# Kernel optimization log

Hardware: AMD Instinct MI355X
Metric: run time of the kernel (lower is better)

Reference implementation:

```python
import jax, jax.numpy as jnp
import numpy as np

B, N, D, H, DH, L = 2, 1024, 1024, 16, 64, 6
INNER = D * 4 * 2 // 3  # GEGLU inner dim = 2730
SCALE = DH ** -0.5


def _ln(x, g, b):
    m = jnp.mean(x, -1, keepdims=True)
    v = jnp.var(x, -1, keepdims=True)
    return (x - m) / jnp.sqrt(v + 1e-5) * g + b


def _stable_softmax(t, alpha=1024.0):  # alpha = 32**2
    t = t / alpha
    t = t - jax.lax.stop_gradient(jnp.max(t, -1, keepdims=True))
    return jax.nn.softmax(t * alpha, axis=-1)


def setup_inputs() -> dict:
    key = jax.random.key(0)
    ks = jax.random.split(key, 10)
    rn = lambda k, s, sc=0.02: jax.random.normal(k, s, jnp.float32) * sc
    return {
        'x': jax.random.normal(ks[0], (B, N, D), jnp.float32),
        'attn_pre_g': jnp.ones((L, D)), 'attn_pre_b': jnp.zeros((L, D)),
        'attn_post_g': jnp.ones((L, D)), 'attn_post_b': jnp.zeros((L, D)),
        'Wq': rn(ks[1], (L, D, H * DH)), 'Wkv': rn(ks[2], (L, D, 2 * H * DH)),
        'Wo': rn(ks[3], (L, H * DH, D)), 'bo': jnp.zeros((L, D)),
        'null_k': rn(ks[4], (L, H, DH), 1.0), 'null_v': rn(ks[5], (L, H, DH), 1.0),
        'talk': rn(ks[6], (L, H, H), H ** -0.5),
        'ff_pre_g': jnp.ones((L, D)), 'ff_pre_b': jnp.zeros((L, D)),
        'ff_post_g': jnp.ones((L, D)), 'ff_post_b': jnp.zeros((L, D)),
        'W1': rn(ks[7], (L, D, 2 * INNER)), 'b1': jnp.zeros((L, 2 * INNER)),
        'W2': rn(ks[8], (L, INNER, D)), 'b2': jnp.zeros((L, D)),
        'final_g': jnp.ones((D,)), 'final_b': jnp.zeros((D,)),
    }


def _forward(x, attn_pre_g, attn_pre_b, attn_post_g, attn_post_b, Wq, Wkv, Wo, bo,
             null_k, null_v, talk, ff_pre_g, ff_pre_b, ff_post_g, ff_post_b,
             W1, b1, W2, b2, final_g, final_b):
    b, n, _ = x.shape
    neg = -jnp.finfo(x.dtype).max
    causal = jnp.triu(jnp.ones((n, n + 1), bool), 2)  # null kv slot at j=0 never masked
    for l in range(L):
        # --- talking-heads attention, sandwich-normed ---
        h = _ln(x, attn_pre_g[l], attn_pre_b[l])
        q = (h @ Wq[l]).reshape(b, n, H, DH).transpose(0, 2, 1, 3)
        k, v = jnp.split(h @ Wkv[l], 2, -1)
        k = k.reshape(b, n, H, DH).transpose(0, 2, 1, 3)
        v = v.reshape(b, n, H, DH).transpose(0, 2, 1, 3)
        nk = jnp.broadcast_to(null_k[l][None, :, None, :], (b, H, 1, DH))
        nv = jnp.broadcast_to(null_v[l][None, :, None, :], (b, H, 1, DH))
        k = jnp.concatenate([nk, k], 2)  # [b,H,n+1,DH]
        v = jnp.concatenate([nv, v], 2)
        sim = jnp.einsum('bhid,bhjd->bhij', q * SCALE, k)
        sim = jnp.where(causal, neg, sim)
        a = _stable_softmax(sim)
        a = jnp.einsum('gh,bhij->bgij', talk[l], a)  # 1x1 Conv2d over head channel
        o = jnp.einsum('bhij,bhjd->bhid', a, v).transpose(0, 2, 1, 3).reshape(b, n, H * DH)
        o = o @ Wo[l] + bo[l]
        x = x + _ln(o, attn_post_g[l], attn_post_b[l])
        # --- GEGLU feedforward, sandwich-normed ---
        h = _ln(x, ff_pre_g[l], ff_pre_b[l])
        u = h @ W1[l] + b1[l]
        ua, ug = jnp.split(u, 2, -1)
        o = (ua * jax.nn.gelu(ug, approximate=False)) @ W2[l] + b2[l]
        x = x + _ln(o, ff_post_g[l], ff_post_b[l])
    # StableLayerNorm
    x = x / jax.lax.stop_gradient(jnp.max(x, -1, keepdims=True))
    return _ln(x, final_g, final_b)


def reference(x, attn_pre_g, attn_pre_b, attn_post_g, attn_post_b, Wq, Wkv, Wo, bo,
              null_k, null_v, talk, ff_pre_g, ff_pre_b, ff_post_g, ff_post_b,
              W1, b1, W2, b2, final_g, final_b):
    return _forward(x, attn_pre_g, attn_pre_b, attn_post_g, attn_post_b, Wq, Wkv, Wo, bo,
                    null_k, null_v, talk, ff_pre_g, ff_pre_b, ff_post_g, ff_post_b,
                    W1, b1, W2, b2, final_g, final_b)
```

## Files before the change

### kernel.cpp

```cpp
#include <hip/hip_runtime.h>
#include <hip/hip_bf16.h>
#include <float.h>
#include <math.h>


#define N_SEQ 1024
#define DMODEL 1024
#define NH 16
#define DH 64
#define NLAYER 6
#define FF_INNER 2730
#define K2PAD 2752
#define PSTRIDE 1028

typedef float f32x4 __attribute__((ext_vector_type(4)));
typedef short s16x8 __attribute__((ext_vector_type(8)));
typedef unsigned long long u64;

__device__ __forceinline__ ushort f2bf(float f) {
  return __builtin_bit_cast(ushort, __float2bfloat16(f));
}
__device__ __forceinline__ u64 pack4(float a, float b, float c, float d) {
  return (u64)f2bf(a) | ((u64)f2bf(b) << 16) | ((u64)f2bf(c) << 32) |
         ((u64)f2bf(d) << 48);
}
#define GLD_LDS16(g, l)                                                        \
  __builtin_amdgcn_global_load_lds(                                            \
      (const __attribute__((address_space(1))) void*)(g),                      \
      (__attribute__((address_space(3))) void*)(l), 16, 0, 0)

__device__ __forceinline__ float wave_sum(float v) {
#pragma unroll
  for (int o = 32; o > 0; o >>= 1) v += __shfl_xor(v, o, 64);
  return v;
}
__device__ __forceinline__ float wave_max(float v) {
#pragma unroll
  for (int o = 32; o > 0; o >>= 1) v = fmaxf(v, __shfl_xor(v, o, 64));
  return v;
}
__device__ __forceinline__ float block_sum(float v, float* s) {
  v = wave_sum(v);
  __syncthreads();
  if ((threadIdx.x & 63) == 0) s[threadIdx.x >> 6] = v;
  __syncthreads();
  return s[0] + s[1] + s[2] + s[3];
}
__device__ __forceinline__ float block_max(float v, float* s) {
  v = wave_max(v);
  __syncthreads();
  if ((threadIdx.x & 63) == 0) s[threadIdx.x >> 6] = v;
  __syncthreads();
  return fmaxf(fmaxf(s[0], s[1]), fmaxf(s[2], s[3]));
}

__global__ __launch_bounds__(256) void ln_res_kernel(const float* __restrict__ in,
                                                     const float* __restrict__ gw,
                                                     const float* __restrict__ bw,
                                                     float* __restrict__ out) {
  __shared__ float red[4];
  const int row = blockIdx.x, t = threadIdx.x;
  float4 v = *(const float4*)(in + (size_t)row * DMODEL + t * 4);
  float mean = block_sum(v.x + v.y + v.z + v.w, red) * (1.0f / DMODEL);
  float4 d = make_float4(v.x - mean, v.y - mean, v.z - mean, v.w - mean);
  float var = block_sum(d.x * d.x + d.y * d.y + d.z * d.z + d.w * d.w, red) * (1.0f / DMODEL);
  float rstd = rsqrtf(var + 1e-5f);
  float4 g4 = *(const float4*)(gw + t * 4);
  float4 b4 = *(const float4*)(bw + t * 4);
  float* q = out + (size_t)row * DMODEL + t * 4;
  float4 xv = *(float4*)q;
  xv.x += d.x * rstd * g4.x + b4.x;
  xv.y += d.y * rstd * g4.y + b4.y;
  xv.z += d.z * rstd * g4.z + b4.z;
  xv.w += d.w * rstd * g4.w + b4.w;
  *(float4*)q = xv;
}

__global__ __launch_bounds__(256) void ln_bf16_kernel(const float* __restrict__ in,
                                                      const float* __restrict__ gw,
                                                      const float* __restrict__ bw,
                                                      ushort* __restrict__ out) {
  __shared__ float red[4];
  const int row = blockIdx.x, t = threadIdx.x;
  float4 v = *(const float4*)(in + (size_t)row * DMODEL + t * 4);
  float mean = block_sum(v.x + v.y + v.z + v.w, red) * (1.0f / DMODEL);
  float4 d = make_float4(v.x - mean, v.y - mean, v.z - mean, v.w - mean);
  float var = block_sum(d.x * d.x + d.y * d.y + d.z * d.z + d.w * d.w, red) * (1.0f / DMODEL);
  float rstd = rsqrtf(var + 1e-5f);
  float4 g4 = *(const float4*)(gw + t * 4);
  float4 b4 = *(const float4*)(bw + t * 4);
  *(u64*)(out + (size_t)row * DMODEL + t * 4) =
      pack4(d.x * rstd * g4.x + b4.x, d.y * rstd * g4.y + b4.y,
            d.z * rstd * g4.z + b4.z, d.w * rstd * g4.w + b4.w);
}

__global__ __launch_bounds__(256) void final_kernel(const float* __restrict__ in,
                                                    const float* __restrict__ gw,
                                                    const float* __restrict__ bw,
                                                    float* __restrict__ out) {
  __shared__ float red[4];
  const int row = blockIdx.x, t = threadIdx.x;
  float4 v = *(const float4*)(in + (size_t)row * DMODEL + t * 4);
  float mx = block_max(fmaxf(fmaxf(v.x, v.y), fmaxf(v.z, v.w)), red);
  float4 y = make_float4(v.x / mx, v.y / mx, v.z / mx, v.w / mx);
  float mean = block_sum(y.x + y.y + y.z + y.w, red) * (1.0f / DMODEL);
  float4 d = make_float4(y.x - mean, y.y - mean, y.z - mean, y.w - mean);
  float var = block_sum(d.x * d.x + d.y * d.y + d.z * d.z + d.w * d.w, red) * (1.0f / DMODEL);
  float rstd = rsqrtf(var + 1e-5f);
  float4 g4 = *(const float4*)(gw + t * 4);
  float4 b4 = *(const float4*)(bw + t * 4);
  float4 r = make_float4(d.x * rstd * g4.x + b4.x, d.y * rstd * g4.y + b4.y,
                         d.z * rstd * g4.z + b4.z, d.w * rstd * g4.w + b4.w);
  *(float4*)(out + (size_t)row * DMODEL + t * 4) = r;
}

__global__ __launch_bounds__(256) void cvtT_kernel(const float* __restrict__ W,
                                                   ushort* __restrict__ Wt,
                                                   int K, int N, int Kpad) {
  __shared__ float tile[32][33];
  const int n0 = blockIdx.x * 32, k0 = blockIdx.y * 32;
  const int tr = threadIdx.x >> 3, tc4 = (threadIdx.x & 7) * 4;
  int gk = k0 + tr;
  float4 v = make_float4(0, 0, 0, 0);
  if (gk < K) {
    if (n0 + tc4 + 3 < N) {
      v = *(const float4*)(W + (size_t)gk * N + n0 + tc4);
    } else {
      if (n0 + tc4 + 0 < N) v.x = W[(size_t)gk * N + n0 + tc4 + 0];
      if (n0 + tc4 + 1 < N) v.y = W[(size_t)gk * N + n0 + tc4 + 1];
      if (n0 + tc4 + 2 < N) v.z = W[(size_t)gk * N + n0 + tc4 + 2];
      if (n0 + tc4 + 3 < N) v.w = W[(size_t)gk * N + n0 + tc4 + 3];
    }
  }
  tile[tr][tc4 + 0] = v.x; tile[tr][tc4 + 1] = v.y;
  tile[tr][tc4 + 2] = v.z; tile[tr][tc4 + 3] = v.w;
  __syncthreads();
  *(u64*)(Wt + (size_t)(n0 + tr) * Kpad + k0 + tc4) =
      pack4(tile[tc4 + 0][tr], tile[tc4 + 1][tr], tile[tc4 + 2][tr], tile[tc4 + 3][tr]);
}

__global__ __launch_bounds__(256) void gemm_bf16(const ushort* __restrict__ A,
                                                 const ushort* __restrict__ Bt,
                                                 const float* __restrict__ bias,
                                                 float* __restrict__ C,
                                                 int N, int K, int lda, int ldb) {
  __shared__ __align__(16) ushort Al[128 * 32];
  __shared__ __align__(16) ushort Bl[128 * 32];
  const int n0 = blockIdx.x * 128, m0 = blockIdx.y * 128;
  const int t = threadIdx.x, lane = t & 63, w = t >> 6;
  const int wm = w >> 1, wn = w & 1;

  f32x4 acc[4][4];
#pragma unroll
  for (int i = 0; i < 4; i++)
#pragma unroll
    for (int j = 0; j < 4; j++) acc[i][j] = (f32x4){0.f, 0.f, 0.f, 0.f};

  const int sm = t >> 2, sk = (t & 3) * 8;
  const ushort* ga0 = A + (size_t)(m0 + sm) * lda + sk;
  const ushort* ga1 = ga0 + (size_t)64 * lda;
  const ushort* gb0 = Bt + (size_t)(n0 + sm) * ldb + sk;
  const ushort* gb1 = gb0 + (size_t)64 * ldb;
  ushort* la0 = &Al[t * 8];
  ushort* la1 = &Al[2048 + t * 8];
  ushort* lb0 = &Bl[t * 8];
  ushort* lb1 = &Bl[2048 + t * 8];

  const int kk = (lane >> 4) * 8;
  const int rA = wm * 64 + (lane & 15);
  const int rB = wn * 64 + (lane & 15);

  for (int k0 = 0; k0 < K; k0 += 32) {
    GLD_LDS16(ga0 + k0, la0);
    GLD_LDS16(ga1 + k0, la1);
    GLD_LDS16(gb0 + k0, lb0);
    GLD_LDS16(gb1 + k0, lb1);
    __syncthreads();
    s16x8 fa[4], fb[4];
#pragma unroll
    for (int mi = 0; mi < 4; mi++)
      fa[mi] = *(const s16x8*)&Al[(rA + mi * 16) * 32 + kk];
#pragma unroll
    for (int ni = 0; ni < 4; ni++)
      fb[ni] = *(const s16x8*)&Bl[(rB + ni * 16) * 32 + kk];
#pragma unroll
    for (int mi = 0; mi < 4; mi++)
#pragma unroll
      for (int ni = 0; ni < 4; ni++)
        acc[mi][ni] = __builtin_amdgcn_mfma_f32_16x16x32_bf16(
            fa[mi], fb[ni], acc[mi][ni], 0, 0, 0);
    __syncthreads();
  }

  const int crow = m0 + wm * 64 + (lane >> 4) * 4;
  const int ccol = n0 + wn * 64 + (lane & 15);
#pragma unroll
  for (int ni = 0; ni < 4; ni++) {
    int gc = ccol + ni * 16;
    if (gc >= N) continue;
    float bv = bias ? bias[gc] : 0.f;
#pragma unroll
    for (int mi = 0; mi < 4; mi++)
#pragma unroll
      for (int r = 0; r < 4; r++)
        C[(size_t)(crow + mi * 16 + r) * N + gc] = acc[mi][ni][r] + bv;
  }
}

__global__ __launch_bounds__(256) void scores_kernel(const float* __restrict__ q,
                                                     const float* __restrict__ kv,
                                                     const float* __restrict__ nullk,
                                                     float* __restrict__ probs, int b) {
  __shared__ float Qs[64][68];
  __shared__ float Ks[64][68];
  const int h = blockIdx.z, i0 = blockIdx.y * 64, j0 = blockIdx.x * 64;
  const int t = threadIdx.x, tx = t & 15, ty = t >> 4;
#pragma unroll
  for (int r = 0; r < 4; r++) {
    int f = t + r * 256;
    int i = f >> 4, d4 = (f & 15) << 2;
    float4 v = *(const float4*)(q + ((size_t)(b * N_SEQ) + i0 + i) * DMODEL + h * DH + d4);
    Qs[d4 + 0][i] = v.x; Qs[d4 + 1][i] = v.y; Qs[d4 + 2][i] = v.z; Qs[d4 + 3][i] = v.w;
  }
#pragma unroll
  for (int r = 0; r < 4; r++) {
    int f = t + r * 256;
    int j = f >> 4, d4 = (f & 15) << 2;
    int jg = j0 + j;
    float4 v = make_float4(0, 0, 0, 0);
    if (jg == 0)
      v = *(const float4*)(nullk + h * DH + d4);
    else if (jg < N_SEQ + 1)
      v = *(const float4*)(kv + ((size_t)(b * N_SEQ) + jg - 1) * 2048 + h * DH + d4);
    Ks[d4 + 0][j] = v.x; Ks[d4 + 1][j] = v.y; Ks[d4 + 2][j] = v.z; Ks[d4 + 3][j] = v.w;
  }
  __syncthreads();
  float acc[4][4];
#pragma unroll
  for (int i = 0; i < 4; i++)
#pragma unroll
    for (int j = 0; j < 4; j++) acc[i][j] = 0.f;
#pragma unroll 16
  for (int d = 0; d < 64; d++) {
    float av[4], bv[4];
    *(float4*)av = *(const float4*)&Qs[d][ty * 4];
    *(float4*)bv = *(const float4*)&Ks[d][tx * 4];
#pragma unroll
    for (int i = 0; i < 4; i++)
#pragma unroll
      for (int j = 0; j < 4; j++) acc[i][j] = fmaf(av[i], bv[j], acc[i][j]);
  }
#pragma unroll
  for (int ii = 0; ii < 4; ii++) {
    int i = i0 + ty * 4 + ii;
#pragma unroll
    for (int jj = 0; jj < 4; jj++) {
      int j = j0 + tx * 4 + jj;
      if (j < N_SEQ + 1) {
        float s = acc[ii][jj] * 0.125f;
        if (j > i + 1) s = -FLT_MAX;
        probs[((size_t)h * N_SEQ + i) * PSTRIDE + j] = s;
      }
    }
  }
}

__global__ __launch_bounds__(256) void softmax_kernel(float* __restrict__ probs) {
  __shared__ float red[4];
  const int row = blockIdx.x;
  float* p = probs + (size_t)row * PSTRIDE;
  const int t = threadIdx.x;
  float v[5];
#pragma unroll
  for (int c = 0; c < 5; c++) {
    int j = t + c * 256;
    v[c] = (j < N_SEQ + 1) ? p[j] : -FLT_MAX;
  }
  float m = fmaxf(fmaxf(fmaxf(v[0], v[1]), fmaxf(v[2], v[3])), v[4]);
  m = block_max(m, red);
  float s = 0.f;
#pragma unroll
  for (int c = 0; c < 5; c++) {
    v[c] = expf(v[c] - m);
    s += v[c];
  }
  s = block_sum(s, red);
#pragma unroll
  for (int c = 0; c < 5; c++) {
    int j = t + c * 256;
    if (j < N_SEQ + 1) p[j] = v[c] / s;
  }
}

__global__ __launch_bounds__(256) void mix_kernel(float* __restrict__ probs,
                                                  const float* __restrict__ talk) {
  __shared__ float tk[256];
  const int i = blockIdx.x;
  tk[threadIdx.x] = talk[threadIdx.x];
  __syncthreads();
  for (int j = threadIdx.x; j < N_SEQ + 1; j += 256) {
    float a[16];
#pragma unroll
    for (int hh = 0; hh < 16; hh++) a[hh] = probs[((size_t)hh * N_SEQ + i) * PSTRIDE + j];
#pragma unroll
    for (int g = 0; g < 16; g++) {
      float s = 0.f;
#pragma unroll
      for (int hh = 0; hh < 16; hh++) s = fmaf(tk[g * 16 + hh], a[hh], s);
      probs[((size_t)g * N_SEQ + i) * PSTRIDE + j] = s;
    }
  }
}

__global__ __launch_bounds__(256) void av_kernel(const float* __restrict__ probs,
                                                 const float* __restrict__ kv,
                                                 const float* __restrict__ nullv,
                                                 ushort* __restrict__ o, int b) {
  __shared__ float Ps[32][68];
  __shared__ float Vs[32][68];
  const int h = blockIdx.y, i0 = blockIdx.x * 64;
  const int t = threadIdx.x, tx = t & 15, ty = t >> 4;
  float acc[4][4];
#pragma unroll
  for (int i = 0; i < 4; i++)
#pragma unroll
    for (int j = 0; j < 4; j++) acc[i][j] = 0.f;

  for (int j0 = 0; j0 < N_SEQ + 1; j0 += 32) {
#pragma unroll
    for (int r = 0; r < 2; r++) {
      int f = t + r * 256;
      int i = f >> 3, j4 = (f & 7) << 2;
      const float* src = probs + ((size_t)h * N_SEQ + i0 + i) * PSTRIDE + j0 + j4;
      float e[4];
      if (j0 + j4 + 3 < N_SEQ + 1) {
        float4 v = *(const float4*)src;
        e[0] = v.x; e[1] = v.y; e[2] = v.z; e[3] = v.w;
      } else {
#pragma unroll
        for (int c = 0; c < 4; c++) e[c] = (j0 + j4 + c < N_SEQ + 1) ? src[c] : 0.f;
      }
      Ps[j4 + 0][i] = e[0]; Ps[j4 + 1][i] = e[1]; Ps[j4 + 2][i] = e[2]; Ps[j4 + 3][i] = e[3];
    }
#pragma unroll
    for (int r = 0; r < 2; r++) {
      int f = t + r * 256;
      int j = f >> 4, d4 = (f & 15) << 2;
      int jg = j0 + j;
      float4 v = make_float4(0, 0, 0, 0);
      if (jg == 0)
        v = *(const float4*)(nullv + h * DH + d4);
      else if (jg < N_SEQ + 1)
        v = *(const float4*)(kv + ((size_t)(b * N_SEQ) + jg - 1) * 2048 + 1024 + h * DH + d4);
      *(float4*)&Vs[j][d4] = v;
    }
    __syncthreads();
#pragma unroll 8
    for (int jj = 0; jj < 32; jj++) {
      float av[4], bv[4];
      *(float4*)av = *(const float4*)&Ps[jj][ty * 4];
      *(float4*)bv = *(const float4*)&Vs[jj][tx * 4];
#pragma unroll
      for (int i = 0; i < 4; i++)
#pragma unroll
        for (int j = 0; j < 4; j++) acc[i][j] = fmaf(av[i], bv[j], acc[i][j]);
    }
    __syncthreads();
  }
#pragma unroll
  for (int ii = 0; ii < 4; ii++) {
    *(u64*)(o + ((size_t)(b * N_SEQ) + i0 + ty * 4 + ii) * DMODEL + h * DH + tx * 4) =
        pack4(acc[ii][0], acc[ii][1], acc[ii][2], acc[ii][3]);
  }
}

__global__ __launch_bounds__(256) void geglu_kernel(const float* __restrict__ u,
                                                    ushort* __restrict__ gg) {
  const int i = blockIdx.y;
  const int j = blockIdx.x * 256 + threadIdx.x;
  if (j < K2PAD) {
    float r = 0.f;
    if (j < FF_INNER) {
      float a = u[(size_t)i * (2 * FF_INNER) + j];
      float x = u[(size_t)i * (2 * FF_INNER) + FF_INNER + j];
      r = a * 0.5f * x * (1.0f + erff(x * 0.70710678118654752f));
    }
    gg[(size_t)i * K2PAD + j] = f2bf(r);
  }
}

extern "C" void kernel_launch(void* const* d_in, const int* in_sizes, int n_in,
                              void* d_out, int out_size, void* d_ws, size_t ws_size,
                              hipStream_t stream) {
  const float* xin        = (const float*)d_in[0];
  const float* attn_pre_g = (const float*)d_in[1];
  const float* attn_pre_b = (const float*)d_in[2];
  const float* attn_post_g= (const float*)d_in[3];
  const float* attn_post_b= (const float*)d_in[4];
  const float* Wq         = (const float*)d_in[5];
  const float* Wkv        = (const float*)d_in[6];
  const float* Wo         = (const float*)d_in[7];
  const float* bo         = (const float*)d_in[8];
  const float* null_k     = (const float*)d_in[9];
  const float* null_v     = (const float*)d_in[10];
  const float* talk       = (const float*)d_in[11];
  const float* ff_pre_g   = (const float*)d_in[12];
  const float* ff_pre_b   = (const float*)d_in[13];
  const float* ff_post_g  = (const float*)d_in[14];
  const float* ff_post_b  = (const float*)d_in[15];
  const float* W1         = (const float*)d_in[16];
  const float* b1         = (const float*)d_in[17];
  const float* W2         = (const float*)d_in[18];
  const float* b2         = (const float*)d_in[19];
  const float* final_g    = (const float*)d_in[20];
  const float* final_b    = (const float*)d_in[21];

  if (ws_size < (size_t)29425664 * sizeof(float)) return;

  float* ws = (float*)d_ws;
  float*  X   = ws;
  ushort* Hbf = (ushort*)(X + (size_t)2097152);
  float*  Q   = (float*)(Hbf) + 1048576;
  float*  KV  = Q + (size_t)2097152;
  ushort* Obf = (ushort*)(KV + (size_t)4194304);
  float*  P2  = (float*)(Obf) + 1048576;
  float*  PR  = P2 + (size_t)2097152;
  float*  PROBS = PR;
  float*  U     = PR;
  ushort* GGbf  = (ushort*)(PR + 11182080);
  ushort* Wt    = (ushort*)(PR + 14000128);

  hipMemcpyAsync(X, xin, (size_t)2097152 * sizeof(float),
                 hipMemcpyDeviceToDevice, stream);

  dim3 blk(256);
  for (int l = 0; l < NLAYER; l++) {
    ln_bf16_kernel<<<2048, blk, 0, stream>>>(X, attn_pre_g + l * 1024, attn_pre_b + l * 1024, Hbf);
    cvtT_kernel<<<dim3(32, 32), blk, 0, stream>>>(Wq + (size_t)l * 1048576, Wt, 1024, 1024, 1024);
    gemm_bf16<<<dim3(8, 16), blk, 0, stream>>>(Hbf, Wt, nullptr, Q, 1024, 1024, 1024, 1024);
    cvtT_kernel<<<dim3(64, 32), blk, 0, stream>>>(Wkv + (size_t)l * 2097152, Wt, 1024, 2048, 1024);
    gemm_bf16<<<dim3(16, 16), blk, 0, stream>>>(Hbf, Wt, nullptr, KV, 2048, 1024, 1024, 1024);
    for (int b = 0; b < 2; b++) {
      scores_kernel<<<dim3(17, 16, 16), blk, 0, stream>>>(Q, KV, null_k + l * NH * DH, PROBS, b);
      softmax_kernel<<<16384, blk, 0, stream>>>(PROBS);
      mix_kernel<<<1024, blk, 0, stream>>>(PROBS, talk + l * 256);
      av_kernel<<<dim3(16, 16), blk, 0, stream>>>(PROBS, KV, null_v + l * NH * DH, Obf, b);
    }
    cvtT_kernel<<<dim3(32, 32), blk, 0, stream>>>(Wo + (size_t)l * 1048576, Wt, 1024, 1024, 1024);
    gemm_bf16<<<dim3(8, 16), blk, 0, stream>>>(Obf, Wt, bo + l * 1024, P2, 1024, 1024, 1024, 1024);
    ln_res_kernel<<<2048, blk, 0, stream>>>(P2, attn_post_g + l * 1024, attn_post_b + l * 1024, X);

    ln_bf16_kernel<<<2048, blk, 0, stream>>>(X, ff_pre_g + l * 1024, ff_pre_b + l * 1024, Hbf);
    cvtT_kernel<<<dim3(172, 32), blk, 0, stream>>>(W1 + (size_t)l * 5591040, Wt, 1024, 5460, 1024);
    gemm_bf16<<<dim3(43, 16), blk, 0, stream>>>(Hbf, Wt, b1 + l * 5460, U, 5460, 1024, 1024, 1024);
    geglu_kernel<<<dim3(11, 2048), blk, 0, stream>>>(U, GGbf);
    cvtT_kernel<<<dim3(32, 86), blk, 0, stream>>>(W2 + (size_t)l * 2795520, Wt, 2730, 1024, K2PAD);
    gemm_bf16<<<dim3(8, 16), blk, 0, stream>>>(GGbf, Wt, b2 + l * 1024, P2, 1024, K2PAD, K2PAD, K2PAD);
    ln_res_kernel<<<2048, blk, 0, stream>>>(P2, ff_post_g + l * 1024, ff_post_b + l * 1024, X);
  }
  final_kernel<<<2048, blk, 0, stream>>>(X, final_g, final_b, (float*)d_out);
}
```

Before: 3.978 ms.

## Move attention to bf16 MFMA with fused causal softmax and talking-heads mix

```diff
diff --git a/kernel.cpp b/kernel.cpp
--- a/kernel.cpp
+++ b/kernel.cpp
@@ -6,12 +6,12 @@
 
 #define N_SEQ 1024
 #define DMODEL 1024
-#define NH 16
-#define DH 64
 #define NLAYER 6
 #define FF_INNER 2730
 #define K2PAD 2752
-#define PSTRIDE 1028
+#define PSTR 1028
+#define PBSTR 1056
+#define KHROWS 1152
 
 typedef float f32x4 __attribute__((ext_vector_type(4)));
 typedef short s16x8 __attribute__((ext_vector_type(8)));
@@ -19,6 +19,9 @@
 
 __device__ __forceinline__ ushort f2bf(float f) {
   return __builtin_bit_cast(ushort, __float2bfloat16(f));
+}
+__device__ __forceinline__ float bf2f(ushort u) {
+  union { unsigned i; float f; } x; x.i = ((unsigned)u) << 16; return x.f;
 }
 __device__ __forceinline__ u64 pack4(float a, float b, float c, float d) {
   return (u64)f2bf(a) | ((u64)f2bf(b) << 16) | ((u64)f2bf(c) << 32) |
@@ -139,10 +142,11 @@
       pack4(tile[tc4 + 0][tr], tile[tc4 + 1][tr], tile[tc4 + 2][tr], tile[tc4 + 3][tr]);
 }
 
+template <int OBF>
 __global__ __launch_bounds__(256) void gemm_bf16(const ushort* __restrict__ A,
                                                  const ushort* __restrict__ Bt,
                                                  const float* __restrict__ bias,
-                                                 float* __restrict__ C,
+                                                 void* __restrict__ Cv,
                                                  int N, int K, int lda, int ldb) {
   __shared__ __align__(16) ushort Al[128 * 32];
   __shared__ __align__(16) ushort Bl[128 * 32];
@@ -202,187 +206,244 @@
 #pragma unroll
     for (int mi = 0; mi < 4; mi++)
 #pragma unroll
-      for (int r = 0; r < 4; r++)
-        C[(size_t)(crow + mi * 16 + r) * N + gc] = acc[mi][ni][r] + bv;
-  }
-}
-
-__global__ __launch_bounds__(256) void scores_kernel(const float* __restrict__ q,
-                                                     const float* __restrict__ kv,
-                                                     const float* __restrict__ nullk,
-                                                     float* __restrict__ probs, int b) {
-  __shared__ float Qs[64][68];
-  __shared__ float Ks[64][68];
-  const int h = blockIdx.z, i0 = blockIdx.y * 64, j0 = blockIdx.x * 64;
-  const int t = threadIdx.x, tx = t & 15, ty = t >> 4;
-#pragma unroll
-  for (int r = 0; r < 4; r++) {
-    int f = t + r * 256;
-    int i = f >> 4, d4 = (f & 15) << 2;
-    float4 v = *(const float4*)(q + ((size_t)(b * N_SEQ) + i0 + i) * DMODEL + h * DH + d4);
-    Qs[d4 + 0][i] = v.x; Qs[d4 + 1][i] = v.y; Qs[d4 + 2][i] = v.z; Qs[d4 + 3][i] = v.w;
-  }
-#pragma unroll
-  for (int r = 0; r < 4; r++) {
-    int f = t + r * 256;
-    int j = f >> 4, d4 = (f & 15) << 2;
-    int jg = j0 + j;
-    float4 v = make_float4(0, 0, 0, 0);
-    if (jg == 0)
-      v = *(const float4*)(nullk + h * DH + d4);
-    else if (jg < N_SEQ + 1)
-      v = *(const float4*)(kv + ((size_t)(b * N_SEQ) + jg - 1) * 2048 + h * DH + d4);
-    Ks[d4 + 0][j] = v.x; Ks[d4 + 1][j] = v.y; Ks[d4 + 2][j] = v.z; Ks[d4 + 3][j] = v.w;
-  }
-  __syncthreads();
-  float acc[4][4];
+      for (int r = 0; r < 4; r++) {
+        float val = acc[mi][ni][r] + bv;
+        size_t off = (size_t)(crow + mi * 16 + r) * N + gc;
+        if (OBF) ((ushort*)Cv)[off] = f2bf(val);
+        else     ((float*)Cv)[off]  = val;
+      }
+  }
+}
+
+__global__ __launch_bounds__(256) void prep_kv(const ushort* __restrict__ KVbf,
+                                               const float* __restrict__ nk,
+                                               const float* __restrict__ nv,
+                                               ushort* __restrict__ Kh,
+                                               ushort* __restrict__ Vt) {
+  const int b = blockIdx.x >> 4, h = blockIdx.x & 15;
+  const int t = threadIdx.x;
+  ushort* khb = Kh + (size_t)(b * 16 + h) * KHROWS * 64;
+  for (int idx = t; idx < KHROWS * 16; idx += 256) {
+    int j = idx >> 4, c4 = (idx & 15) * 4;
+    u64 v = 0;
+    if (j == 0) {
+      v = pack4(nk[h * 64 + c4], nk[h * 64 + c4 + 1],
+                nk[h * 64 + c4 + 2], nk[h * 64 + c4 + 3]);
+    } else if (j <= N_SEQ) {
+      v = *(const u64*)&KVbf[(size_t)(b * N_SEQ + j - 1) * 2048 + h * 64 + c4];
+    }
+    *(u64*)&khb[j * 64 + c4] = v;
+  }
+  ushort* vtb = Vt + (size_t)(b * 16 + h) * 64 * PBSTR;
+  for (int idx = t; idx < PBSTR * 16; idx += 256) {
+    int j = idx >> 4, d4 = (idx & 15) * 4;
+    ushort e0 = 0, e1 = 0, e2 = 0, e3 = 0;
+    if (j == 0) {
+      e0 = f2bf(nv[h * 64 + d4]);     e1 = f2bf(nv[h * 64 + d4 + 1]);
+      e2 = f2bf(nv[h * 64 + d4 + 2]); e3 = f2bf(nv[h * 64 + d4 + 3]);
+    } else if (j <= N_SEQ) {
+      u64 v = *(const u64*)&KVbf[(size_t)(b * N_SEQ + j - 1) * 2048 + 1024 + h * 64 + d4];
+      e0 = (ushort)v; e1 = (ushort)(v >> 16); e2 = (ushort)(v >> 32); e3 = (ushort)(v >> 48);
+    }
+    vtb[(d4 + 0) * PBSTR + j] = e0;
+    vtb[(d4 + 1) * PBSTR + j] = e1;
+    vtb[(d4 + 2) * PBSTR + j] = e2;
+    vtb[(d4 + 3) * PBSTR + j] = e3;
+  }
+}
+
+__global__ __launch_bounds__(256) void scores_mfma(const ushort* __restrict__ Qbf,
+                                                   const ushort* __restrict__ Kh,
+                                                   float* __restrict__ probs,
+                                                   int b, int ihalf) {
+  const int tj = blockIdx.x, til = blockIdx.y, h = blockIdx.z;
+  const int ti = ihalf * 4 + til;
+  const int m0 = ti * 128, n0 = tj * 128;
+  if (n0 > m0 + 128) return;
+  __shared__ __align__(16) ushort Al[128 * 32];
+  __shared__ __align__(16) ushort Bl[128 * 32];
+  const int t = threadIdx.x, lane = t & 63, w = t >> 6;
+  const int wm = w >> 1, wn = w & 1;
+
+  f32x4 acc[4][4];
 #pragma unroll
   for (int i = 0; i < 4; i++)
 #pragma unroll
-    for (int j = 0; j < 4; j++) acc[i][j] = 0.f;
-#pragma unroll 16
-  for (int d = 0; d < 64; d++) {
-    float av[4], bv[4];
-    *(float4*)av = *(const float4*)&Qs[d][ty * 4];
-    *(float4*)bv = *(const float4*)&Ks[d][tx * 4];
-#pragma unroll
-    for (int i = 0; i < 4; i++)
-#pragma unroll
-      for (int j = 0; j < 4; j++) acc[i][j] = fmaf(av[i], bv[j], acc[i][j]);
-  }
-#pragma unroll
-  for (int ii = 0; ii < 4; ii++) {
-    int i = i0 + ty * 4 + ii;
-#pragma unroll
-    for (int jj = 0; jj < 4; jj++) {
-      int j = j0 + tx * 4 + jj;
-      if (j < N_SEQ + 1) {
-        float s = acc[ii][jj] * 0.125f;
-        if (j > i + 1) s = -FLT_MAX;
-        probs[((size_t)h * N_SEQ + i) * PSTRIDE + j] = s;
+    for (int j = 0; j < 4; j++) acc[i][j] = (f32x4){0.f, 0.f, 0.f, 0.f};
+
+  const int sm = t >> 2, sk = (t & 3) * 8;
+  const ushort* ga0 = Qbf + (size_t)(b * N_SEQ + m0 + sm) * DMODEL + h * 64 + sk;
+  const ushort* ga1 = ga0 + (size_t)64 * DMODEL;
+  const ushort* gb0 = Kh + ((size_t)(b * 16 + h) * KHROWS + n0 + sm) * 64 + sk;
+  const ushort* gb1 = gb0 + (size_t)64 * 64;
+  ushort* la0 = &Al[t * 8];
+  ushort* la1 = &Al[2048 + t * 8];
+  ushort* lb0 = &Bl[t * 8];
+  ushort* lb1 = &Bl[2048 + t * 8];
+
+  const int kk = (lane >> 4) * 8;
+  const int rA = wm * 64 + (lane & 15);
+  const int rB = wn * 64 + (lane & 15);
+
+#pragma unroll
+  for (int k0 = 0; k0 < 64; k0 += 32) {
+    GLD_LDS16(ga0 + k0, la0);
+    GLD_LDS16(ga1 + k0, la1);
+    GLD_LDS16(gb0 + k0, lb0);
+    GLD_LDS16(gb1 + k0, lb1);
+    __syncthreads();
+    s16x8 fa[4], fb[4];
+#pragma unroll
+    for (int mi = 0; mi < 4; mi++)
+      fa[mi] = *(const s16x8*)&Al[(rA + mi * 16) * 32 + kk];
+#pragma unroll
+    for (int ni = 0; ni < 4; ni++)
+      fb[ni] = *(const s16x8*)&Bl[(rB + ni * 16) * 32 + kk];
+#pragma unroll
+    for (int mi = 0; mi < 4; mi++)
+#pragma unroll
+      for (int ni = 0; ni < 4; ni++)
+        acc[mi][ni] = __builtin_amdgcn_mfma_f32_16x16x32_bf16(
+            fa[mi], fb[ni], acc[mi][ni], 0, 0, 0);
+    __syncthreads();
+  }
+
+  const int crow = m0 + wm * 64 + (lane >> 4) * 4;
+  const int ccol = n0 + wn * 64 + (lane & 15);
+#pragma unroll
+  for (int ni = 0; ni < 4; ni++) {
+    int gc = ccol + ni * 16;
+    if (gc >= PSTR) continue;
+#pragma unroll
+    for (int mi = 0; mi < 4; mi++)
+#pragma unroll
+      for (int r = 0; r < 4; r++) {
+        int ig = crow + mi * 16 + r;
+        probs[((size_t)h * 512 + (ig & 511)) * PSTR + gc] = acc[mi][ni][r] * 0.125f;
+      }
+  }
+}
+
+__global__ __launch_bounds__(256) void smmix_kernel(const float* __restrict__ probs,
+                                                    const float* __restrict__ talk,
+                                                    ushort* __restrict__ PB, int ihalf) {
+  __shared__ __align__(16) float sl[16][PSTR];
+  __shared__ float tk[16][16];
+  __shared__ float ms[16], rls[16];
+  const int il = blockIdx.x;
+  const int ig = ihalf * 512 + il;
+  const int jmax = ig + 2;
+  const int t = threadIdx.x;
+  tk[t >> 4][t & 15] = talk[t];
+  const int nch = (jmax + 3) >> 2;
+  for (int idx = t; idx < 16 * nch; idx += 256) {
+    int h = idx / nch, c = idx - h * nch;
+    *(float4*)&sl[h][c * 4] = *(const float4*)&probs[((size_t)h * 512 + il) * PSTR + c * 4];
+  }
+  __syncthreads();
+  {
+    const int h = t >> 4, l16 = t & 15;
+    float m = -FLT_MAX;
+    for (int j = l16; j < jmax; j += 16) m = fmaxf(m, sl[h][j]);
+#pragma unroll
+    for (int o = 1; o < 16; o <<= 1) m = fmaxf(m, __shfl_xor(m, o, 16));
+    float s = 0.f;
+    for (int j = l16; j < jmax; j += 16) s += expf(sl[h][j] - m);
+#pragma unroll
+    for (int o = 1; o < 16; o <<= 1) s += __shfl_xor(s, o, 16);
+    if (l16 == 0) { ms[h] = m; rls[h] = 1.0f / s; }
+  }
+  __syncthreads();
+  for (int idx = t; idx < 16 * 257; idx += 256) {
+    int h = idx / 257, c = idx - h * 257;
+    float4 v = *(float4*)&sl[h][c * 4];
+    float m = ms[h], rl = rls[h];
+    int j = c * 4;
+    v.x = (j + 0 < jmax) ? expf(v.x - m) * rl : 0.f;
+    v.y = (j + 1 < jmax) ? expf(v.y - m) * rl : 0.f;
+    v.z = (j + 2 < jmax) ? expf(v.z - m) * rl : 0.f;
+    v.w = (j + 3 < jmax) ? expf(v.w - m) * rl : 0.f;
+    *(float4*)&sl[h][c * 4] = v;
+  }
+  __syncthreads();
+  for (int idx = t; idx < 16 * (PBSTR / 4); idx += 256) {
+    int g = idx / (PBSTR / 4), c = idx - g * (PBSTR / 4);
+    float ax = 0.f, ay = 0.f, az = 0.f, aw = 0.f;
+    if (c < 257) {
+#pragma unroll
+      for (int h = 0; h < 16; h++) {
+        float4 p = *(float4*)&sl[h][c * 4];
+        float wgh = tk[g][h];
+        ax += wgh * p.x; ay += wgh * p.y; az += wgh * p.z; aw += wgh * p.w;
       }
     }
-  }
-}
-
-__global__ __launch_bounds__(256) void softmax_kernel(float* __restrict__ probs) {
-  __shared__ float red[4];
-  const int row = blockIdx.x;
-  float* p = probs + (size_t)row * PSTRIDE;
-  const int t = threadIdx.x;
-  float v[5];
-#pragma unroll
-  for (int c = 0; c < 5; c++) {
-    int j = t + c * 256;
-    v[c] = (j < N_SEQ + 1) ? p[j] : -FLT_MAX;
-  }
-  float m = fmaxf(fmaxf(fmaxf(v[0], v[1]), fmaxf(v[2], v[3])), v[4]);
-  m = block_max(m, red);
-  float s = 0.f;
-#pragma unroll
-  for (int c = 0; c < 5; c++) {
-    v[c] = expf(v[c] - m);
-    s += v[c];
-  }
-  s = block_sum(s, red);
-#pragma unroll
-  for (int c = 0; c < 5; c++) {
-    int j = t + c * 256;
-    if (j < N_SEQ + 1) p[j] = v[c] / s;
-  }
-}
-
-__global__ __launch_bounds__(256) void mix_kernel(float* __restrict__ probs,
-                                                  const float* __restrict__ talk) {
-  __shared__ float tk[256];
-  const int i = blockIdx.x;
-  tk[threadIdx.x] = talk[threadIdx.x];
-  __syncthreads();
-  for (int j = threadIdx.x; j < N_SEQ + 1; j += 256) {
-    float a[16];
-#pragma unroll
-    for (int hh = 0; hh < 16; hh++) a[hh] = probs[((size_t)hh * N_SEQ + i) * PSTRIDE + j];
-#pragma unroll
-    for (int g = 0; g < 16; g++) {
-      float s = 0.f;
-#pragma unroll
-      for (int hh = 0; hh < 16; hh++) s = fmaf(tk[g * 16 + hh], a[hh], s);
-      probs[((size_t)g * N_SEQ + i) * PSTRIDE + j] = s;
-    }
-  }
-}
-
-__global__ __launch_bounds__(256) void av_kernel(const float* __restrict__ probs,
-                                                 const float* __restrict__ kv,
-                                                 const float* __restrict__ nullv,
-                                                 ushort* __restrict__ o, int b) {
-  __shared__ float Ps[32][68];
-  __shared__ float Vs[32][68];
-  const int h = blockIdx.y, i0 = blockIdx.x * 64;
-  const int t = threadIdx.x, tx = t & 15, ty = t >> 4;
-  float acc[4][4];
-#pragma unroll
-  for (int i = 0; i < 4; i++)
-#pragma unroll
-    for (int j = 0; j < 4; j++) acc[i][j] = 0.f;
-
-  for (int j0 = 0; j0 < N_SEQ + 1; j0 += 32) {
-#pragma unroll
-    for (int r = 0; r < 2; r++) {
-      int f = t + r * 256;
-      int i = f >> 3, j4 = (f & 7) << 2;
-      const float* src = probs + ((size_t)h * N_SEQ + i0 + i) * PSTRIDE + j0 + j4;
-      float e[4];
-      if (j0 + j4 + 3 < N_SEQ + 1) {
-        float4 v = *(const float4*)src;
-        e[0] = v.x; e[1] = v.y; e[2] = v.z; e[3] = v.w;
-      } else {
-#pragma unroll
-        for (int c = 0; c < 4; c++) e[c] = (j0 + j4 + c < N_SEQ + 1) ? src[c] : 0.f;
-      }
-      Ps[j4 + 0][i] = e[0]; Ps[j4 + 1][i] = e[1]; Ps[j4 + 2][i] = e[2]; Ps[j4 + 3][i] = e[3];
-    }
-#pragma unroll
-    for (int r = 0; r < 2; r++) {
-      int f = t + r * 256;
-      int j = f >> 4, d4 = (f & 15) << 2;
-      int jg = j0 + j;
-      float4 v = make_float4(0, 0, 0, 0);
-      if (jg == 0)
-        v = *(const float4*)(nullv + h * DH + d4);
-      else if (jg < N_SEQ + 1)
-        v = *(const float4*)(kv + ((size_t)(b * N_SEQ) + jg - 1) * 2048 + 1024 + h * DH + d4);
-      *(float4*)&Vs[j][d4] = v;
-    }
+    *(u64*)&PB[((size_t)g * N_SEQ + ig) * PBSTR + c * 4] = pack4(ax, ay, az, aw);
+  }
+}
+
+__global__ __launch_bounds__(256) void av_mfma(const ushort* __restrict__ PB,
+                                               const ushort* __restrict__ Vt,
+                                               ushort* __restrict__ Obf, int b) {
+  __shared__ __align__(16) ushort Al[64 * 32];
+  __shared__ __align__(16) ushort Bl[64 * 32];
+  const int m0 = blockIdx.x * 64, g = blockIdx.y;
+  const int t = threadIdx.x, lane = t & 63, w = t >> 6;
+  const int wm = w >> 1, wn = w & 1;
+  f32x4 acc[2][2];
+#pragma unroll
+  for (int i = 0; i < 2; i++)
+#pragma unroll
+    for (int j = 0; j < 2; j++) acc[i][j] = (f32x4){0.f, 0.f, 0.f, 0.f};
+
+  const int sm = t >> 2, sk = (t & 3) * 8;
+  const ushort* ga = PB + ((size_t)g * N_SEQ + m0 + sm) * PBSTR + sk;
+  const ushort* gb = Vt + ((size_t)(b * 16 + g) * 64 + sm) * PBSTR + sk;
+  ushort* la = &Al[t * 8];
+  ushort* lb = &Bl[t * 8];
+
+  const int kk = (lane >> 4) * 8;
+  const int rA = wm * 32 + (lane & 15);
+  const int rB = wn * 32 + (lane & 15);
+
+  for (int k0 = 0; k0 < PBSTR; k0 += 32) {
+    GLD_LDS16(ga + k0, la);
+    GLD_LDS16(gb + k0, lb);
     __syncthreads();
-#pragma unroll 8
-    for (int jj = 0; jj < 32; jj++) {
-      float av[4], bv[4];
-      *(float4*)av = *(const float4*)&Ps[jj][ty * 4];
-      *(float4*)bv = *(const float4*)&Vs[jj][tx * 4];
-#pragma unroll
-      for (int i = 0; i < 4; i++)
-#pragma unroll
-        for (int j = 0; j < 4; j++) acc[i][j] = fmaf(av[i], bv[j], acc[i][j]);
-    }
+    s16x8 fa[2], fb[2];
+    fa[0] = *(const s16x8*)&Al[rA * 32 + kk];
+    fa[1] = *(const s16x8*)&Al[(rA + 16) * 32 + kk];
+    fb[0] = *(const s16x8*)&Bl[rB * 32 + kk];
+    fb[1] = *(const s16x8*)&Bl[(rB + 16) * 32 + kk];
+#pragma unroll
+    for (int mi = 0; mi < 2; mi++)
+#pragma unroll
+      for (int ni = 0; ni < 2; ni++)
+        acc[mi][ni] = __builtin_amdgcn_mfma_f32_16x16x32_bf16(
+            fa[mi], fb[ni], acc[mi][ni], 0, 0, 0);
     __syncthreads();
   }
-#pragma unroll
-  for (int ii = 0; ii < 4; ii++) {
-    *(u64*)(o + ((size_t)(b * N_SEQ) + i0 + ty * 4 + ii) * DMODEL + h * DH + tx * 4) =
-        pack4(acc[ii][0], acc[ii][1], acc[ii][2], acc[ii][3]);
-  }
-}
-
-__global__ __launch_bounds__(256) void geglu_kernel(const float* __restrict__ u,
+
+  const int crow = m0 + wm * 32 + (lane >> 4) * 4;
+  const int ccol = wn * 32 + (lane & 15);
+#pragma unroll
+  for (int ni = 0; ni < 2; ni++)
+#pragma unroll
+    for (int mi = 0; mi < 2; mi++)
+#pragma unroll
+      for (int r = 0; r < 4; r++)
+        Obf[(size_t)(b * N_SEQ + crow + mi * 16 + r) * DMODEL + g * 64 + ccol + ni * 16] =
+            f2bf(acc[mi][ni][r]);
+}
+
+__global__ __launch_bounds__(256) void geglu_kernel(const ushort* __restrict__ u,
                                                     ushort* __restrict__ gg) {
   const int i = blockIdx.y;
   const int j = blockIdx.x * 256 + threadIdx.x;
   if (j < K2PAD) {
     float r = 0.f;
     if (j < FF_INNER) {
-      float a = u[(size_t)i * (2 * FF_INNER) + j];
-      float x = u[(size_t)i * (2 * FF_INNER) + FF_INNER + j];
+      float a = bf2f(u[(size_t)i * (2 * FF_INNER) + j]);
+      float x = bf2f(u[(size_t)i * (2 * FF_INNER) + FF_INNER + j]);
       r = a * 0.5f * x * (1.0f + erff(x * 0.70710678118654752f));
     }
     gg[(size_t)i * K2PAD + j] = f2bf(r);
@@ -415,20 +476,23 @@
   const float* final_g    = (const float*)d_in[20];
   const float* final_b    = (const float*)d_in[21];
 
-  if (ws_size < (size_t)29425664 * sizeof(float)) return;
+  if (ws_size < (size_t)28217344 * sizeof(float)) return;
 
   float* ws = (float*)d_ws;
-  float*  X   = ws;
-  ushort* Hbf = (ushort*)(X + (size_t)2097152);
-  float*  Q   = (float*)(Hbf) + 1048576;
-  float*  KV  = Q + (size_t)2097152;
-  ushort* Obf = (ushort*)(KV + (size_t)4194304);
-  float*  P2  = (float*)(Obf) + 1048576;
-  float*  PR  = P2 + (size_t)2097152;
-  float*  PROBS = PR;
-  float*  U     = PR;
-  ushort* GGbf  = (ushort*)(PR + 11182080);
-  ushort* Wt    = (ushort*)(PR + 14000128);
+  float*  X    = ws;
+  ushort* Hbf  = (ushort*)(ws + 2097152);
+  ushort* Obf  = Hbf;
+  ushort* Qbf  = (ushort*)(ws + 3145728);
+  ushort* KVbf = (ushort*)(ws + 4194304);
+  ushort* PB   = (ushort*)(ws + 4194304);
+  float*  P2   = ws + 12632064;
+  ushort* Kh   = (ushort*)(ws + 14729216);
+  ushort* Vt   = (ushort*)(ws + 15908864);
+  float*  BIG  = ws + 16990208;
+  float*  PROBS = BIG;
+  ushort* Ubf   = (ushort*)BIG;
+  ushort* GGbf  = (ushort*)(BIG + 5591040);
+  ushort* Wt    = (ushort*)(BIG + 8409088);
 
   hipMemcpyAsync(X, xin, (size_t)2097152 * sizeof(float),
                  hipMemcpyDeviceToDevice, stream);
@@ -437,25 +501,27 @@
   for (int l = 0; l < NLAYER; l++) {
     ln_bf16_kernel<<<2048, blk, 0, stream>>>(X, attn_pre_g + l * 1024, attn_pre_b + l * 1024, Hbf);
     cvtT_kernel<<<dim3(32, 32), blk, 0, stream>>>(Wq + (size_t)l * 1048576, Wt, 1024, 1024, 1024);
-    gemm_bf16<<<dim3(8, 16), blk, 0, stream>>>(Hbf, Wt, nullptr, Q, 1024, 1024, 1024, 1024);
+    gemm_bf16<1><<<dim3(8, 16), blk, 0, stream>>>(Hbf, Wt, nullptr, Qbf, 1024, 1024, 1024, 1024);
     cvtT_kernel<<<dim3(64, 32), blk, 0, stream>>>(Wkv + (size_t)l * 2097152, Wt, 1024, 2048, 1024);
-    gemm_bf16<<<dim3(16, 16), blk, 0, stream>>>(Hbf, Wt, nullptr, KV, 2048, 1024, 1024, 1024);
+    gemm_bf16<1><<<dim3(16, 16), blk, 0, stream>>>(Hbf, Wt, nullptr, KVbf, 2048, 1024, 1024, 1024);
+    prep_kv<<<32, blk, 0, stream>>>(KVbf, null_k + l * 1024, null_v + l * 1024, Kh, Vt);
     for (int b = 0; b < 2; b++) {
-      scores_kernel<<<dim3(17, 16, 16), blk, 0, stream>>>(Q, KV, null_k + l * NH * DH, PROBS, b);
-      softmax_kernel<<<16384, blk, 0, stream>>>(PROBS);
-      mix_kernel<<<1024, blk, 0, stream>>>(PROBS, talk + l * 256);
-      av_kernel<<<dim3(16, 16), blk, 0, stream>>>(PROBS, KV, null_v + l * NH * DH, Obf, b);
+      for (int ih = 0; ih < 2; ih++) {
+        scores_mfma<<<dim3(9, 4, 16), blk, 0, stream>>>(Qbf, Kh, PROBS, b, ih);
+        smmix_kernel<<<512, blk, 0, stream>>>(PROBS, talk + l * 256, PB, ih);
+      }
+      av_mfma<<<dim3(16, 16), blk, 0, stream>>>(PB, Vt, Obf, b);
     }
     cvtT_kernel<<<dim3(32, 32), blk, 0, stream>>>(Wo + (size_t)l * 1048576, Wt, 1024, 1024, 1024);
-    gemm_bf16<<<dim3(8, 16), blk, 0, stream>>>(Obf, Wt, bo + l * 1024, P2, 1024, 1024, 1024, 1024);
+    gemm_bf16<0><<<dim3(8, 16), blk, 0, stream>>>(Obf, Wt, bo + l * 1024, P2, 1024, 1024, 1024, 1024);
     ln_res_kernel<<<2048, blk, 0, stream>>>(P2, attn_post_g + l * 1024, attn_post_b + l * 1024, X);
 
     ln_bf16_kernel<<<2048, blk, 0, stream>>>(X, ff_pre_g + l * 1024, ff_pre_b + l * 1024, Hbf);
     cvtT_kernel<<<dim3(172, 32), blk, 0, stream>>>(W1 + (size_t)l * 5591040, Wt, 1024, 5460, 1024);
-    gemm_bf16<<<dim3(43, 16), blk, 0, stream>>>(Hbf, Wt, b1 + l * 5460, U, 5460, 1024, 1024, 1024);
-    geglu_kernel<<<dim3(11, 2048), blk, 0, stream>>>(U, GGbf);
+    gemm_bf16<1><<<dim3(43, 16), blk, 0, stream>>>(Hbf, Wt, b1 + l * 5460, Ubf, 5460, 1024, 1024, 1024);
+    geglu_kernel<<<dim3(11, 2048), blk, 0, stream>>>(Ubf, GGbf);
     cvtT_kernel<<<dim3(32, 86), blk, 0, stream>>>(W2 + (size_t)l * 2795520, Wt, 2730, 1024, K2PAD);
-    gemm_bf16<<<dim3(8, 16), blk, 0, stream>>>(GGbf, Wt, b2 + l * 1024, P2, 1024, K2PAD, K2PAD, K2PAD);
+    gemm_bf16<0><<<dim3(8, 16), blk, 0, stream>>>(GGbf, Wt, b2 + l * 1024, P2, 1024, K2PAD, K2PAD, K2PAD);
     ln_res_kernel<<<2048, blk, 0, stream>>>(P2, ff_post_g + l * 1024, ff_post_b + l * 1024, X);
   }
   final_kernel<<<2048, blk, 0, stream>>>(X, final_g, final_b, (float*)d_out);
```

After: 3.233 ms. 1.23x faster.
